# Performance work log

Measured on AMD Instinct MI355X. Metric: run time of the kernel, lower is better.

## Reference

```python
import jax, jax.numpy as jnp
import numpy as np

B, N, D = 4, 4096, 3
Q = jnp.array([0.05, 0.95, 0.25, 0.75], dtype=jnp.float32)  # q_begin + q_end


def _nn_diff(S1, S2):
    # For each point in S1 find nearest point in S2 (squared L2), return S1 - closest_S2.
    # d2: [N, N] built via the ||a||^2 + ||b||^2 - 2ab expansion (avoids [N,N,D]).
    d2 = (jnp.sum(S1 * S1, axis=-1, keepdims=True)
          + jnp.sum(S2 * S2, axis=-1)[None, :]
          - 2.0 * (S1 @ S2.T))
    idx = jnp.argmin(d2, axis=1)          # [N] nearest index in S2
    return S1 - S2[idx]                   # [N, D] vector residuals (mean=False path)


def _masked_std(v, mask):
    # torch.std over the masked subset (unbiased, correction=1), mask is float {0,1}.
    n = jnp.sum(mask)
    mean = jnp.sum(v * mask) / n
    var = jnp.sum(mask * (v - mean) ** 2) / (n - 1.0)
    return jnp.sqrt(var)


def _mask_std_pair(d):
    # mask_by_Z: quantiles computed under no_grad (stop_gradient), then std of each subset.
    v = d.reshape(-1)
    q = jnp.quantile(jax.lax.stop_gradient(v), Q.astype(v.dtype))
    mask_begin = ((v < q[0]) | (v > q[1])).astype(v.dtype)
    mask_end = ((v > q[2]) & (v < q[3])).astype(v.dtype)
    return _masked_std(v, mask_begin), _masked_std(v, mask_end)


def _sigma_distance(S1, S2):
    d12 = _nn_diff(S1, S2)  # S1 -> S2 residuals
    d21 = _nn_diff(S2, S1)  # S2 -> S1 residuals
    b1, e1 = _mask_std_pair(d12)
    b2, e2 = _mask_std_pair(d21)
    return jnp.maximum(b1, b2), jnp.maximum(e1, e2)


def setup_inputs() -> dict:
    key = jax.random.key(0)
    kx, ky = jax.random.split(key)
    x = jax.random.normal(kx, (B, N, D), dtype=jnp.float32)
    y = jax.random.normal(ky, (B, N, D), dtype=jnp.float32)
    return {"x": x, "y": y}


def reference(x, y):
    begin, end = jax.vmap(_sigma_distance)(x, y)  # [B], [B]
    return begin.mean(), end.mean()
```

## Files before the change

### kernel.cpp

```cpp
#include <hip/hip_runtime.h>
#include <math.h>

constexpr int B_  = 4;
constexpr int N_  = 4096;
constexpr int NV  = N_ * 3;
constexpr int QPT = 8;

__device__ inline unsigned f2k(float f) {
    unsigned b = __float_as_uint(f);
    return b ^ ((unsigned)((int)b >> 31) | 0x80000000u);
}
__device__ inline float k2f(unsigned k) {
    unsigned b = (k & 0x80000000u) ? (k ^ 0x80000000u) : ~k;
    return __uint_as_float(b);
}

__global__ __launch_bounds__(256) void nn_partial_kernel(const float* __restrict__ x,
                                                         const float* __restrict__ y,
                                                         float2* __restrict__ part,
                                                         int ncch) {
    __shared__ float4 s2[1024];
    const int cch  = N_ / ncch;
    const int pair = blockIdx.z;
    const int b    = pair >> 1;
    const int dir  = pair & 1;
    const float* S1 = (dir == 0 ? x : y) + b * NV;
    const float* S2 = (dir == 0 ? y : x) + b * NV;
    const int cbase = blockIdx.x * cch;

    for (int j = threadIdx.x; j < cch; j += 256) {
        float bx = S2[(cbase + j) * 3 + 0];
        float by = S2[(cbase + j) * 3 + 1];
        float bz = S2[(cbase + j) * 3 + 2];
        s2[j] = make_float4(-2.f * bx, -2.f * by, -2.f * bz,
                            bx * bx + by * by + bz * bz);
    }
    __syncthreads();

    const int q0 = blockIdx.y * 2048 + threadIdx.x * QPT;
    float ax[QPT], ay[QPT], az[QPT];
    {
        const float4* p4 = (const float4*)(S1 + q0 * 3);
        float4 v[6];
        #pragma unroll
        for (int i = 0; i < 6; ++i) v[i] = p4[i];
        const float* f = (const float*)v;
        #pragma unroll
        for (int k = 0; k < QPT; ++k) {
            ax[k] = f[k * 3 + 0]; ay[k] = f[k * 3 + 1]; az[k] = f[k * 3 + 2];
        }
    }

    float best[QPT]; int idx[QPT];
    #pragma unroll
    for (int k = 0; k < QPT; ++k) { best[k] = INFINITY; idx[k] = 0; }

    #pragma unroll 2
    for (int j = 0; j < cch; ++j) {
        float4 c = s2[j];
        const int jg = cbase + j;
        #pragma unroll
        for (int k = 0; k < QPT; ++k) {
            float d2 = fmaf(ax[k], c.x, fmaf(ay[k], c.y, fmaf(az[k], c.z, c.w)));
            if (d2 < best[k]) idx[k] = jg;
            best[k] = fminf(d2, best[k]);
        }
    }

    float2 o[QPT];
    #pragma unroll
    for (int k = 0; k < QPT; ++k) o[k] = make_float2(best[k], (float)idx[k]);
    float4* op = (float4*)(part + (size_t)(pair * ncch + blockIdx.x) * N_ + q0);
    #pragma unroll
    for (int i = 0; i < QPT / 2; ++i) op[i] = ((const float4*)o)[i];
}

__global__ __launch_bounds__(256) void nn_merge_kernel(const float* __restrict__ x,
                                                       const float* __restrict__ y,
                                                       const float2* __restrict__ part,
                                                       float* __restrict__ resid,
                                                       int ncch) {
    const int pair = blockIdx.y;
    const int b    = pair >> 1;
    const int dir  = pair & 1;
    const float* S1 = (dir == 0 ? x : y) + b * NV;
    const float* S2 = (dir == 0 ? y : x) + b * NV;
    const int q = blockIdx.x * 256 + threadIdx.x;

    float best = INFINITY;
    int bidx = 0;
    for (int c = 0; c < ncch; ++c) {
        float2 p = part[(size_t)(pair * ncch + c) * N_ + q];
        if (p.x < best) { best = p.x; bidx = (int)p.y; }
    }
    float* outp = resid + pair * NV + q * 3;
    outp[0] = S1[q * 3 + 0] - S2[bidx * 3 + 0];
    outp[1] = S1[q * 3 + 1] - S2[bidx * 3 + 1];
    outp[2] = S1[q * 3 + 2] - S2[bidx * 3 + 2];
}

__global__ __launch_bounds__(256) void quantile_select_kernel(const float* __restrict__ resid,
                                                              float* __restrict__ qbuf) {
    __shared__ unsigned keys[NV];
    __shared__ int hist[256];
    __shared__ int s_sel, s_want, s_cnt;
    __shared__ unsigned s_min;

    const int t    = blockIdx.x & 3;
    const int pair = blockIdx.x >> 2;
    const int tid  = threadIdx.x;
    const int lane = tid & 63;

    const float Qs[4] = {0.05f, 0.95f, 0.25f, 0.75f};
    const float pos = Qs[t] * (float)(NV - 1);
    const int   k0  = (int)floorf(pos);
    const float fr  = pos - (float)k0;

    const float4* v4 = (const float4*)(resid + pair * NV);
    for (int i = tid; i < NV / 4; i += 256) {
        float4 v = v4[i];
        uint4 k = make_uint4(f2k(v.x), f2k(v.y), f2k(v.z), f2k(v.w));
        ((uint4*)keys)[i] = k;
    }
    __syncthreads();

    unsigned prefix = 0u, pmask = 0u;
    int want = k0;
    for (int shift = 24; shift >= 0; shift -= 8) {
        hist[tid] = 0;
        __syncthreads();
        for (int i = tid; i < NV; i += 256) {
            unsigned k = keys[i];
            if ((k & pmask) == prefix) atomicAdd(&hist[(k >> shift) & 255], 1);
        }
        __syncthreads();
        if (tid < 64) {
            int c0 = hist[tid * 4 + 0], c1 = hist[tid * 4 + 1];
            int c2 = hist[tid * 4 + 2], c3 = hist[tid * 4 + 3];
            int s = c0 + c1 + c2 + c3;
            int pre = s;
            #pragma unroll
            for (int off = 1; off < 64; off <<= 1) {
                int u = __shfl_up(pre, off);
                if (tid >= off) pre += u;
            }
            int excl = pre - s;
            bool hit = (want >= excl) && (want < excl + s);
            unsigned long long m = __ballot(hit);
            int hl = (int)(__ffsll((unsigned long long)m) - 1);
            if (tid == hl) {
                int w = want - excl;
                int sel;
                if      (w < c0)           { sel = tid * 4 + 0; }
                else if (w < c0 + c1)      { sel = tid * 4 + 1; w -= c0; }
                else if (w < c0 + c1 + c2) { sel = tid * 4 + 2; w -= c0 + c1; }
                else                       { sel = tid * 4 + 3; w -= c0 + c1 + c2; }
                s_sel = sel; s_want = w;
            }
        }
        __syncthreads();
        prefix |= ((unsigned)s_sel) << shift;
        pmask  |= (0xFFu << shift);
        want = s_want;
        __syncthreads();
    }
    const unsigned key0 = prefix;
    const float v0 = k2f(key0);

    if (tid == 0) { s_cnt = 0; s_min = 0xFFFFFFFFu; }
    __syncthreads();
    int loc = 0; unsigned locmin = 0xFFFFFFFFu;
    for (int i = tid; i < NV; i += 256) {
        unsigned k = keys[i];
        if (k <= key0) loc++;
        else if (k < locmin) locmin = k;
    }
    for (int off = 32; off > 0; off >>= 1) {
        loc += __shfl_down(loc, off);
        unsigned m2 = __shfl_down(locmin, off);
        locmin = (m2 < locmin) ? m2 : locmin;
    }
    if (lane == 0) { atomicAdd(&s_cnt, loc); atomicMin(&s_min, locmin); }
    __syncthreads();
    if (tid == 0) {
        float v1 = (s_cnt >= k0 + 2) ? v0 : k2f(s_min);
        qbuf[pair * 4 + t] = v0 + fr * (v1 - v0);
    }
}

__global__ __launch_bounds__(256) void masked_stats_kernel(const float* __restrict__ resid,
                                                           const float* __restrict__ qbuf,
                                                           float* __restrict__ stats) {
    __shared__ float red[16];
    __shared__ float sh[8];
    const int pair = blockIdx.x;
    const int tid  = threadIdx.x;
    const int wid = tid >> 6, lane = tid & 63;
    const float4* v4 = (const float4*)(resid + pair * NV);
    const float q0 = qbuf[pair * 4 + 0], q1 = qbuf[pair * 4 + 1];
    const float q2 = qbuf[pair * 4 + 2], q3 = qbuf[pair * 4 + 3];

    float cb = 0.f, sb = 0.f, ce = 0.f, se = 0.f;
    for (int i = tid; i < NV / 4; i += 256) {
        float4 v = v4[i];
        float vals[4] = {v.x, v.y, v.z, v.w};
        #pragma unroll
        for (int u = 0; u < 4; ++u) {
            float val = vals[u];
            if ((val < q0) || (val > q1)) { cb += 1.f; sb += val; }
            if ((val > q2) && (val < q3)) { ce += 1.f; se += val; }
        }
    }
    for (int off = 32; off > 0; off >>= 1) {
        cb += __shfl_down(cb, off);
        sb += __shfl_down(sb, off);
        ce += __shfl_down(ce, off);
        se += __shfl_down(se, off);
    }
    if (lane == 0) {
        red[wid * 4 + 0] = cb; red[wid * 4 + 1] = sb;
        red[wid * 4 + 2] = ce; red[wid * 4 + 3] = se;
    }
    __syncthreads();
    if (tid == 0) {
        float tcb = 0.f, tsb = 0.f, tce = 0.f, tse = 0.f;
        for (int w = 0; w < 4; ++w) {
            tcb += red[w * 4 + 0]; tsb += red[w * 4 + 1];
            tce += red[w * 4 + 2]; tse += red[w * 4 + 3];
        }
        sh[0] = tsb / tcb;
        sh[1] = tse / tce;
        sh[2] = tcb;
        sh[3] = tce;
    }
    __syncthreads();
    const float mean_b = sh[0], mean_e = sh[1];
    const float nb = sh[2], ne = sh[3];

    float vb = 0.f, ve = 0.f;
    for (int i = tid; i < NV / 4; i += 256) {
        float4 v = v4[i];
        float vals[4] = {v.x, v.y, v.z, v.w};
        #pragma unroll
        for (int u = 0; u < 4; ++u) {
            float val = vals[u];
            if ((val < q0) || (val > q1)) { float d = val - mean_b; vb += d * d; }
            if ((val > q2) && (val < q3)) { float d = val - mean_e; ve += d * d; }
        }
    }
    for (int off = 32; off > 0; off >>= 1) {
        vb += __shfl_down(vb, off);
        ve += __shfl_down(ve, off);
    }
    __syncthreads();
    if (lane == 0) { red[wid * 2 + 0] = vb; red[wid * 2 + 1] = ve; }
    __syncthreads();
    if (tid == 0) {
        float tvb = 0.f, tve = 0.f;
        for (int w = 0; w < 4; ++w) { tvb += red[w * 2 + 0]; tve += red[w * 2 + 1]; }
        stats[pair * 2 + 0] = sqrtf(tvb / (nb - 1.f));
        stats[pair * 2 + 1] = sqrtf(tve / (ne - 1.f));
    }
}

__global__ void final_kernel(const float* __restrict__ stats, float* __restrict__ out) {
    if (threadIdx.x == 0 && blockIdx.x == 0) {
        float sb = 0.f, se = 0.f;
        for (int b = 0; b < B_; ++b) {
            float b1 = stats[(b * 2 + 0) * 2 + 0];
            float b2 = stats[(b * 2 + 1) * 2 + 0];
            float e1 = stats[(b * 2 + 0) * 2 + 1];
            float e2 = stats[(b * 2 + 1) * 2 + 1];
            sb += fmaxf(b1, b2);
            se += fmaxf(e1, e2);
        }
        out[0] = sb / (float)B_;
        out[1] = se / (float)B_;
    }
}

extern "C" void kernel_launch(void* const* d_in, const int* in_sizes, int n_in,
                              void* d_out, int out_size, void* d_ws, size_t ws_size,
                              hipStream_t stream) {
    const float* x = (const float*)d_in[0];
    const float* y = (const float*)d_in[1];
    float* out = (float*)d_out;

    float*  resid = (float*)d_ws;
    float*  qbuf  = resid + 8 * NV;
    float*  stats = qbuf + 32;
    float2* part  = (float2*)(stats + 16 + 16);

    const size_t head = (size_t)(8 * NV + 64) * sizeof(float);
    int ncch = 4;
    for (int c = 32; c >= 4; c >>= 1) {
        size_t need = head + (size_t)8 * c * N_ * sizeof(float2);
        if (ws_size >= need) { ncch = c; break; }
    }

    nn_partial_kernel<<<dim3(ncch, 2, 8), 256, 0, stream>>>(x, y, part, ncch);
    nn_merge_kernel<<<dim3(N_ / 256, 8), 256, 0, stream>>>(x, y, part, resid, ncch);
    quantile_select_kernel<<<32, 256, 0, stream>>>(resid, qbuf);
    masked_stats_kernel<<<8, 256, 0, stream>>>(resid, qbuf, stats);
    final_kernel<<<1, 64, 0, stream>>>(stats, out);
}
```

Measured before the change: 80.33 us.

## Template chunk count, widen quantile select to 512 threads, aggregate histogram atomics

New measurement: 96.18 us. 1.2x slower.

```diff
diff --git a/kernel.cpp b/kernel.cpp
--- a/kernel.cpp
+++ b/kernel.cpp
@@ -15,20 +15,20 @@
     return __uint_as_float(b);
 }
 
+template <int NCCH>
 __global__ __launch_bounds__(256) void nn_partial_kernel(const float* __restrict__ x,
                                                          const float* __restrict__ y,
-                                                         float2* __restrict__ part,
-                                                         int ncch) {
-    __shared__ float4 s2[1024];
-    const int cch  = N_ / ncch;
+                                                         float2* __restrict__ part) {
+    constexpr int CCH = N_ / NCCH;
+    __shared__ float4 s2[CCH];
     const int pair = blockIdx.z;
     const int b    = pair >> 1;
     const int dir  = pair & 1;
     const float* S1 = (dir == 0 ? x : y) + b * NV;
     const float* S2 = (dir == 0 ? y : x) + b * NV;
-    const int cbase = blockIdx.x * cch;
-
-    for (int j = threadIdx.x; j < cch; j += 256) {
+    const int cbase = blockIdx.x * CCH;
+
+    for (int j = threadIdx.x; j < CCH; j += 256) {
         float bx = S2[(cbase + j) * 3 + 0];
         float by = S2[(cbase + j) * 3 + 1];
         float bz = S2[(cbase + j) * 3 + 2];
@@ -56,7 +56,7 @@
     for (int k = 0; k < QPT; ++k) { best[k] = INFINITY; idx[k] = 0; }
 
     #pragma unroll 2
-    for (int j = 0; j < cch; ++j) {
+    for (int j = 0; j < CCH; ++j) {
         float4 c = s2[j];
         const int jg = cbase + j;
         #pragma unroll
@@ -70,16 +70,16 @@
     float2 o[QPT];
     #pragma unroll
     for (int k = 0; k < QPT; ++k) o[k] = make_float2(best[k], (float)idx[k]);
-    float4* op = (float4*)(part + (size_t)(pair * ncch + blockIdx.x) * N_ + q0);
+    float4* op = (float4*)(part + (size_t)(pair * NCCH + blockIdx.x) * N_ + q0);
     #pragma unroll
     for (int i = 0; i < QPT / 2; ++i) op[i] = ((const float4*)o)[i];
 }
 
+template <int NCCH>
 __global__ __launch_bounds__(256) void nn_merge_kernel(const float* __restrict__ x,
                                                        const float* __restrict__ y,
                                                        const float2* __restrict__ part,
-                                                       float* __restrict__ resid,
-                                                       int ncch) {
+                                                       float* __restrict__ resid) {
     const int pair = blockIdx.y;
     const int b    = pair >> 1;
     const int dir  = pair & 1;
@@ -89,8 +89,9 @@
 
     float best = INFINITY;
     int bidx = 0;
-    for (int c = 0; c < ncch; ++c) {
-        float2 p = part[(size_t)(pair * ncch + c) * N_ + q];
+    #pragma unroll
+    for (int c = 0; c < NCCH; ++c) {
+        float2 p = part[(size_t)(pair * NCCH + c) * N_ + q];
         if (p.x < best) { best = p.x; bidx = (int)p.y; }
     }
     float* outp = resid + pair * NV + q * 3;
@@ -99,7 +100,7 @@
     outp[2] = S1[q * 3 + 2] - S2[bidx * 3 + 2];
 }
 
-__global__ __launch_bounds__(256) void quantile_select_kernel(const float* __restrict__ resid,
+__global__ __launch_bounds__(512) void quantile_select_kernel(const float* __restrict__ resid,
                                                               float* __restrict__ qbuf) {
     __shared__ unsigned keys[NV];
     __shared__ int hist[256];
@@ -117,7 +118,7 @@
     const float fr  = pos - (float)k0;
 
     const float4* v4 = (const float4*)(resid + pair * NV);
-    for (int i = tid; i < NV / 4; i += 256) {
+    for (int i = tid; i < NV / 4; i += 512) {
         float4 v = v4[i];
         uint4 k = make_uint4(f2k(v.x), f2k(v.y), f2k(v.z), f2k(v.w));
         ((uint4*)keys)[i] = k;
@@ -127,11 +128,20 @@
     unsigned prefix = 0u, pmask = 0u;
     int want = k0;
     for (int shift = 24; shift >= 0; shift -= 8) {
-        hist[tid] = 0;
+        if (tid < 256) hist[tid] = 0;
         __syncthreads();
-        for (int i = tid; i < NV; i += 256) {
+        for (int i = tid; i < NV; i += 512) {
             unsigned k = keys[i];
-            if ((k & pmask) == prefix) atomicAdd(&hist[(k >> shift) & 255], 1);
+            const bool valid = ((k & pmask) == prefix);
+            const int b9 = valid ? (int)((k >> shift) & 255) : 256;
+            unsigned long long m = ~0ull;
+            #pragma unroll
+            for (int bit = 0; bit < 9; ++bit) {
+                unsigned long long vote = __ballot((b9 >> bit) & 1);
+                m &= ((b9 >> bit) & 1) ? vote : ~vote;
+            }
+            const int leader = (int)(__ffsll(m) - 1);
+            if (valid && lane == leader) atomicAdd(&hist[b9], __popcll(m));
         }
         __syncthreads();
         if (tid < 64) {
@@ -170,7 +180,7 @@
     if (tid == 0) { s_cnt = 0; s_min = 0xFFFFFFFFu; }
     __syncthreads();
     int loc = 0; unsigned locmin = 0xFFFFFFFFu;
-    for (int i = tid; i < NV; i += 256) {
+    for (int i = tid; i < NV; i += 512) {
         unsigned k = keys[i];
         if (k <= key0) loc++;
         else if (k < locmin) locmin = k;
@@ -279,6 +289,17 @@
     }
 }
 
+template <int NCCH>
+static void run_pipeline(const float* x, const float* y, float2* part,
+                         float* resid, float* qbuf, float* stats, float* out,
+                         hipStream_t stream) {
+    nn_partial_kernel<NCCH><<<dim3(NCCH, 2, 8), 256, 0, stream>>>(x, y, part);
+    nn_merge_kernel<NCCH><<<dim3(N_ / 256, 8), 256, 0, stream>>>(x, y, part, resid);
+    quantile_select_kernel<<<32, 512, 0, stream>>>(resid, qbuf);
+    masked_stats_kernel<<<8, 256, 0, stream>>>(resid, qbuf, stats);
+    final_kernel<<<1, 64, 0, stream>>>(stats, out);
+}
+
 extern "C" void kernel_launch(void* const* d_in, const int* in_sizes, int n_in,
                               void* d_out, int out_size, void* d_ws, size_t ws_size,
                               hipStream_t stream) {
@@ -292,15 +313,11 @@
     float2* part  = (float2*)(stats + 16 + 16);
 
     const size_t head = (size_t)(8 * NV + 64) * sizeof(float);
-    int ncch = 4;
-    for (int c = 32; c >= 4; c >>= 1) {
-        size_t need = head + (size_t)8 * c * N_ * sizeof(float2);
-        if (ws_size >= need) { ncch = c; break; }
-    }
-
-    nn_partial_kernel<<<dim3(ncch, 2, 8), 256, 0, stream>>>(x, y, part, ncch);
-    nn_merge_kernel<<<dim3(N_ / 256, 8), 256, 0, stream>>>(x, y, part, resid, ncch);
-    quantile_select_kernel<<<32, 256, 0, stream>>>(resid, qbuf);
-    masked_stats_kernel<<<8, 256, 0, stream>>>(resid, qbuf, stats);
-    final_kernel<<<1, 64, 0, stream>>>(stats, out);
-}
+    const size_t need32 = head + (size_t)8 * 32 * N_ * sizeof(float2);
+
+    if (ws_size >= need32) {
+        run_pipeline<32>(x, y, part, resid, qbuf, stats, out, stream);
+    } else {
+        run_pipeline<4>(x, y, part, resid, qbuf, stats, out, stream);
+    }
+}
```
